# Performance work log

Hardware: AMD Instinct MI355X
Metric: run time of the kernel (lower is better)

The kernel has to match this reference:

```python
import math
import jax, jax.numpy as jnp
import numpy as np

B, NQ, NK, DIM, H, HD = 2, 1024, 2048, 1024, 16, 64


def setup_inputs() -> dict:
    key = jax.random.key(0)
    ks = jax.random.split(key, 12)
    s = 1.0 / math.sqrt(DIM)
    return {
        "q": jax.random.normal(ks[0], (B, NQ, DIM), jnp.float32),
        "k": jax.random.normal(ks[1], (B, NK, DIM), jnp.float32),
        "v": jax.random.normal(ks[2], (B, NK, DIM), jnp.float32),
        "distances": jax.random.uniform(ks[3], (B, NQ, NK), jnp.float32),
        "attn_mask": jax.random.bernoulli(ks[4], 0.5, (B, NQ, NK)),
        "key_padding_mask_q": jax.random.bernoulli(ks[5], 0.5, (B, NQ)),
        "key_padding_mask_k": jax.random.bernoulli(ks[6], 0.5, (B, NK)),
        "Wq": jax.random.normal(ks[7], (H * HD, DIM), jnp.float32) * s,
        "Wk": jax.random.normal(ks[8], (H * HD, DIM), jnp.float32) * s,
        "Wv": jax.random.normal(ks[9], (H * HD, DIM), jnp.float32) * s,
        "Wo": jax.random.normal(ks[10], (DIM, H * HD), jnp.float32) * s,
        "gate_alpha": jnp.float32(0.1),
    }


def reference(q, k, v, distances, attn_mask, key_padding_mask_q,
              key_padding_mask_k, Wq, Wk, Wv, Wo, gate_alpha):
    bsz, q_len, _ = q.shape
    k_len = k.shape[1]
    neg = jnp.finfo(q.dtype).min

    # projections -> (B, H, N, HD)
    qp = (q @ Wq.T).reshape(bsz, q_len, H, HD).transpose(0, 2, 1, 3)
    kp = (k @ Wk.T).reshape(bsz, k_len, H, HD).transpose(0, 2, 1, 3)
    vp = (v @ Wv.T).reshape(bsz, k_len, H, HD).transpose(0, 2, 1, 3)

    scores = jnp.einsum('bhqd,bhkd->bhqk', qp, kp) / math.sqrt(HD)
    scores = jnp.where(attn_mask[:, None, :, :], scores, neg)
    scores = jnp.where(key_padding_mask_k[:, None, None, :], scores, neg)

    attn = jax.nn.softmax(scores, axis=-1)  # (B,H,NQ,NK)

    # distance gating: mask, batch-mean normalize, exponential gate
    d = distances * attn_mask.astype(distances.dtype)
    d = d * key_padding_mask_k[:, None, :].astype(d.dtype)
    mean = d.sum(axis=(-1, -2)) / (q_len * k_len + 1e-6)
    mean = jnp.maximum(mean, 1e-6)[:, None, None]
    d = d / mean
    alpha = jax.nn.softplus(gate_alpha)
    gate = jnp.exp(-alpha * d)[:, None, :, :]  # (B,1,NQ,NK)

    w = attn * gate
    w = w / (w.sum(axis=-1, keepdims=True) + 1e-6)

    out = jnp.einsum('bhqk,bhkd->bhqd', w, vp)
    out = out.transpose(0, 2, 1, 3).reshape(bsz, q_len, H * HD)
    out = out * key_padding_mask_q[:, :, None].astype(out.dtype)
    return out @ Wo.T
```

## Files before the change

kernel.cpp:

```cpp
#include <hip/hip_runtime.h>
#include <hip/hip_bf16.h>
#include <cfloat>

#define B_   2
#define NQ_  1024
#define NK_  2048
#define H_   16
#define HD_  64
#define VPAD 2176
#define GPAD 2112

typedef float  floatx4 __attribute__((ext_vector_type(4)));
typedef __bf16 bf16x8  __attribute__((ext_vector_type(8)));
typedef __bf16 bf16x4  __attribute__((ext_vector_type(4)));

static __device__ __forceinline__ floatx4 mfma16(bf16x8 a, bf16x8 b, floatx4 c) {
    return __builtin_amdgcn_mfma_f32_16x16x32_bf16(a, b, c, 0, 0, 0);
}

static __device__ __forceinline__ void gl_lds(const __bf16* g, __bf16* lbase,
                                              int lane) {
#if __has_builtin(__builtin_amdgcn_global_load_lds)
    __builtin_amdgcn_global_load_lds(
        (const __attribute__((address_space(1))) void*)g,
        (__attribute__((address_space(3))) void*)lbase, 16, 0, 0);
#else
    *(bf16x8*)(lbase + lane * 8) = *(const bf16x8*)g;
#endif
}

struct CvtArgs {
    const float* src[7];
    __bf16*      dst[7];
};

__global__ __launch_bounds__(256) void cvt_mean_kernel(
    CvtArgs a, const float* __restrict__ dist, const int* __restrict__ amask,
    const int* __restrict__ kpmk, float* __restrict__ msum,
    __bf16* __restrict__ dmask)
{
    if (blockIdx.x >= 1792) {
        const int mb = blockIdx.x - 1792;
        const int b  = mb >> 9;
        const float* d  = dist  + (size_t)b * NQ_ * NK_;
        const int*   am = amask + (size_t)b * NQ_ * NK_;
        const int*   km = kpmk  + b * NK_;
        __bf16*      dm = dmask + (size_t)b * NQ_ * GPAD;
        const int base = (mb & 511) * 256 + threadIdx.x;
        float s = 0.f;
        #pragma unroll
        for (int j = 0; j < 4; j++) {
            const int i   = base + j * 131072;
            const int idx = i * 4;
            const int kk  = idx & (NK_ - 1);
            const int q   = i >> 9;
            float4 dv = *(const float4*)(d + idx);
            int4   mv = *(const int4*)(am + idx);
            int4   kv = *(const int4*)(km + kk);
            bf16x4 o;
            if (mv.x && kv.x) { s += dv.x; o[0] = (__bf16)dv.x; } else o[0] = (__bf16)3e38f;
            if (mv.y && kv.y) { s += dv.y; o[1] = (__bf16)dv.y; } else o[1] = (__bf16)3e38f;
            if (mv.z && kv.z) { s += dv.z; o[2] = (__bf16)dv.z; } else o[2] = (__bf16)3e38f;
            if (mv.w && kv.w) { s += dv.w; o[3] = (__bf16)dv.w; } else o[3] = (__bf16)3e38f;
            *(bf16x4*)&dm[(size_t)q * GPAD + kk] = o;
        }
        #pragma unroll
        for (int off = 32; off >= 1; off >>= 1) s += __shfl_down(s, off);
        __shared__ float wsum[4];
        if ((threadIdx.x & 63) == 0) wsum[threadIdx.x >> 6] = s;
        __syncthreads();
        if (threadIdx.x == 0)
            atomicAdd(&msum[b], wsum[0] + wsum[1] + wsum[2] + wsum[3]);
        return;
    }
    #pragma unroll
    for (int j = 0; j < 4; j++) {
        size_t r = (size_t)blockIdx.x * 1024 + j * 256 + threadIdx.x;
        int s;
        if (r < 262144)                  { s = 0; }
        else if ((r -= 262144) < 524288) { s = 1; }
        else if ((r -= 524288) < 524288) { s = 2; }
        else { r -= 524288; s = 3 + (int)(r >> 17); r &= 131071; }
        const float* sp = a.src[s] + r * 8;
        float4 f0 = *(const float4*)sp;
        float4 f1 = *(const float4*)(sp + 4);
        bf16x8 o;
        o[0] = (__bf16)f0.x; o[1] = (__bf16)f0.y; o[2] = (__bf16)f0.z; o[3] = (__bf16)f0.w;
        o[4] = (__bf16)f1.x; o[5] = (__bf16)f1.y; o[6] = (__bf16)f1.z; o[7] = (__bf16)f1.w;
        *(bf16x8*)(a.dst[s] + r * 8) = o;
    }
}

template <typename EPI>
static __device__ __forceinline__ void gemm128_core(
    const __bf16* __restrict__ A, const __bf16* __restrict__ Bw,
    int m0, int n0, __bf16* As, __bf16* Bs, EPI epi)
{
    const int t    = threadIdx.x;
    const int w    = t >> 6, lane = t & 63;
    const int lrow = lane & 15, quad = lane >> 4;
    const int lr   = lane >> 2, lc = lane & 3;

    floatx4 acc[4][4];
    #pragma unroll
    for (int mi = 0; mi < 4; mi++)
        #pragma unroll
        for (int ni = 0; ni < 4; ni++) acc[mi][ni] = floatx4{0.f, 0.f, 0.f, 0.f};

    const __bf16* ga = A  + (size_t)(m0 + w * 32 + lr) * 1024 + lc * 8;
    const __bf16* gb = Bw + (size_t)(n0 + w * 32 + lr) * 1024 + lc * 8;

    for (int k0 = 0; k0 < 1024; k0 += 64) {
        __syncthreads();
        #pragma unroll
        for (int h = 0; h < 2; h++) {
            gl_lds(ga + k0 + h * 32,             &As[h * 4096 + (w * 32) * 32],      lane);
            gl_lds(ga + k0 + h * 32 + 16 * 1024, &As[h * 4096 + (w * 32 + 16) * 32], lane);
            gl_lds(gb + k0 + h * 32,             &Bs[h * 4096 + (w * 32) * 32],      lane);
            gl_lds(gb + k0 + h * 32 + 16 * 1024, &Bs[h * 4096 + (w * 32 + 16) * 32], lane);
        }
        __syncthreads();

        #pragma unroll
        for (int h = 0; h < 2; h++) {
            bf16x8 af[4], bfr[4];
            #pragma unroll
            for (int mi = 0; mi < 4; mi++)
                af[mi] = *(const bf16x8*)
                    &As[h * 4096 + ((w & 1) * 64 + mi * 16 + lrow) * 32 + quad * 8];
            #pragma unroll
            for (int ni = 0; ni < 4; ni++)
                bfr[ni] = *(const bf16x8*)
                    &Bs[h * 4096 + ((w >> 1) * 64 + ni * 16 + lrow) * 32 + quad * 8];
            #pragma unroll
            for (int mi = 0; mi < 4; mi++)
                #pragma unroll
                for (int ni = 0; ni < 4; ni++)
                    acc[mi][ni] = mfma16(af[mi], bfr[ni], acc[mi][ni]);
        }
    }

    #pragma unroll
    for (int mi = 0; mi < 4; mi++)
        #pragma unroll
        for (int ni = 0; ni < 4; ni++)
            #pragma unroll
            for (int r = 0; r < 4; r++) {
                const int m = m0 + (w & 1) * 64 + mi * 16 + quad * 4 + r;
                const int n = n0 + (w >> 1) * 64 + ni * 16 + lrow;
                epi(m, n, acc[mi][ni][r]);
            }
}

template <typename EPI>
static __device__ __forceinline__ void gemm64_core(
    const __bf16* __restrict__ A, const __bf16* __restrict__ Bw,
    int m0, int n0, EPI epi)
{
    __shared__ alignas(16) __bf16 As[2][64 * 32];
    __shared__ alignas(16) __bf16 Bs[2][128 * 32];
    const int t    = threadIdx.x;
    const int w    = t >> 6, lane = t & 63;
    const int lrow = lane & 15, quad = lane >> 4;
    const int lr   = lane >> 2, lc = lane & 3;

    floatx4 acc[4][2];
    #pragma unroll
    for (int mi = 0; mi < 4; mi++)
        #pragma unroll
        for (int ni = 0; ni < 2; ni++) acc[mi][ni] = floatx4{0.f, 0.f, 0.f, 0.f};

    const __bf16* ga = A  + (size_t)(m0 + w * 16 + lr) * 1024 + lc * 8;
    const __bf16* gb = Bw + (size_t)(n0 + w * 32 + lr) * 1024 + lc * 8;

    for (int k0 = 0; k0 < 1024; k0 += 64) {
        __syncthreads();
        #pragma unroll
        for (int h = 0; h < 2; h++) {
            gl_lds(ga + k0 + h * 32,             &As[h][(w * 16) * 32],      lane);
            gl_lds(gb + k0 + h * 32,             &Bs[h][(w * 32) * 32],      lane);
            gl_lds(gb + k0 + h * 32 + 16 * 1024, &Bs[h][(w * 32 + 16) * 32], lane);
        }
        __syncthreads();

        #pragma unroll
        for (int h = 0; h < 2; h++) {
            bf16x8 af[4], bfr[2];
            #pragma unroll
            for (int mi = 0; mi < 4; mi++)
                af[mi] = *(const bf16x8*)
                    &As[h][(mi * 16 + lrow) * 32 + quad * 8];
            #pragma unroll
            for (int ni = 0; ni < 2; ni++)
                bfr[ni] = *(const bf16x8*)
                    &Bs[h][(w * 32 + ni * 16 + lrow) * 32 + quad * 8];
            #pragma unroll
            for (int mi = 0; mi < 4; mi++)
                #pragma unroll
                for (int ni = 0; ni < 2; ni++)
                    acc[mi][ni] = mfma16(af[mi], bfr[ni], acc[mi][ni]);
        }
    }

    #pragma unroll
    for (int mi = 0; mi < 4; mi++)
        #pragma unroll
        for (int ni = 0; ni < 2; ni++)
            #pragma unroll
            for (int r = 0; r < 4; r++) {
                const int m = m0 + mi * 16 + quad * 4 + r;
                const int n = n0 + w * 32 + ni * 16 + lrow;
                epi(m, n, acc[mi][ni][r]);
            }
}

__global__ __launch_bounds__(256) void proj_kernel(
    const __bf16* __restrict__ qb, const __bf16* __restrict__ kb,
    const __bf16* __restrict__ vb, const __bf16* __restrict__ wqb,
    const __bf16* __restrict__ wkb, const __bf16* __restrict__ wvb,
    __bf16* __restrict__ qp, __bf16* __restrict__ kp,
    __bf16* __restrict__ vpT)
{
    __shared__ alignas(16) __bf16 As[2 * 128 * 32];
    __shared__ alignas(16) __bf16 Bs[2 * 128 * 32];
    const int z = blockIdx.z;
    if (z == 0) {
        if ((int)blockIdx.x >= 16) return;
        gemm128_core(qb, wqb, blockIdx.x * 128, blockIdx.y * 128, As, Bs,
                     [&](int m, int n, float v) {
            const int b = m >> 10, q = m & 1023;
            const int h = n >> 6,  d = n & 63;
            qp[(((size_t)(b * 16 + h) * NQ_ + q) << 6) + d] = (__bf16)v;
        });
    } else if (z == 1) {
        gemm128_core(kb, wkb, blockIdx.x * 128, blockIdx.y * 128, As, Bs,
                     [&](int m, int n, float v) {
            const int b = m >> 11, key = m & 2047;
            const int h = n >> 6,  d = n & 63;
            kp[(((size_t)(b * 16 + h) * NK_ + key) << 6) + d] = (__bf16)v;
        });
    } else {
        gemm128_core(wvb, vb, blockIdx.y * 128, blockIdx.x * 128, As, Bs,
                     [&](int m, int n, float v) {
            const int h = m >> 6,  d = m & 63;
            const int b = n >> 11, key = n & 2047;
            vpT[((size_t)(b * 16 + h) * HD_ + d) * VPAD + key] = (__bf16)v;
        });
    }
}

__global__ __launch_bounds__(256) void oproj_kernel(
    const __bf16* __restrict__ A, const __bf16* __restrict__ W,
    float* __restrict__ Cout)
{
    const int m0 = blockIdx.x * 64, n0 = blockIdx.y * 128;
    gemm64_core(A, W, m0, n0, [&](int m, int n, float v) {
        Cout[(size_t)m * 1024 + n] = v;
    });
}

__global__ __launch_bounds__(512, 4) void attn_kernel(
    const __bf16* __restrict__ qp, const __bf16* __restrict__ kp,
    const __bf16* __restrict__ vpT, const __bf16* __restrict__ dmask,
    const float* __restrict__ msum, const float* __restrict__ galpha,
    const int* __restrict__ kpmq, __bf16* __restrict__ attnout)
{
    __shared__ __bf16 Ks[2][64 * 72];
    __shared__ __bf16 Vt[2][64 * 72];
    __shared__ __bf16 Ps[8][16 * 72];
    __shared__ float  Ox[4][16][68];
    __shared__ float  Gx[4][16];
    const int t    = threadIdx.x;
    const int w    = t >> 6, lane = t & 63;
    const int g    = w >> 2;
    const int wg   = w & 3;
    const int lrow = lane & 15, quad = lane >> 4;
    const int qt   = blockIdx.x;
    const int bh   = blockIdx.y;
    const int b    = bh >> 4, h = bh & 15;
    const int q0   = qt * 64 + wg * 16;
    const int k0   = g * (NK_ / 2);
    const int NT   = (NK_ / 2) / 64;

    const float mean  = fmaxf(msum[b] / ((float)(NQ_ * NK_) + 1e-6f), 1e-6f);
    const float alpha = log1pf(__expf(galpha[0]));
    const float cg    = -alpha / mean;

    const __bf16* qb = qp + ((size_t)bh * NQ_ + q0 + lrow) * HD_ + quad * 8;
    const bf16x8 qf0 = *(const bf16x8*)qb;
    const bf16x8 qf1 = *(const bf16x8*)(qb + 32);

    const int tg    = t & 255;
    const int srow0 = tg >> 3,        sc0 = tg & 7;
    const int srow1 = 32 + (tg >> 3), sc1 = tg & 7;
    const int so0 = srow0 * 72 + sc0 * 8;
    const int so1 = srow1 * 72 + sc1 * 8;
    const __bf16* Kg = kp  + (size_t)bh * NK_ * HD_;
    const __bf16* Vg = vpT + (size_t)bh * HD_ * VPAD;
    const __bf16* grow = dmask + ((size_t)b * NQ_ + q0 + lrow) * GPAD;

    float G = 0.f;
    floatx4 O[4];
    #pragma unroll
    for (int nb = 0; nb < 4; nb++) O[nb] = floatx4{0.f, 0.f, 0.f, 0.f};

    bf16x8 kr0, kr1, vr0, vr1;
    bf16x4 gr[4];
    auto loadt = [&](int kb) {
        kr0 = *(const bf16x8*)(Kg + (size_t)(kb + srow0) * HD_ + sc0 * 8);
        kr1 = *(const bf16x8*)(Kg + (size_t)(kb + srow1) * HD_ + sc1 * 8);
        vr0 = *(const bf16x8*)(Vg + (size_t)srow0 * VPAD + kb + sc0 * 8);
        vr1 = *(const bf16x8*)(Vg + (size_t)srow1 * VPAD + kb + sc1 * 8);
        #pragma unroll
        for (int c = 0; c < 4; c++)
            gr[c] = *(const bf16x4*)(grow + kb + c * 16 + quad * 4);
    };
    loadt(k0);

    for (int ib = 0; ib < NT; ib++) {
        const int kb = k0 + ib * 64;

        __syncthreads();
        *(bf16x8*)&Ks[g][so0] = kr0;
        *(bf16x8*)&Ks[g][so1] = kr1;
        *(bf16x8*)&Vt[g][so0] = vr0;
        *(bf16x8*)&Vt[g][so1] = vr1;
        __syncthreads();

        bf16x4 gcur[4];
        #pragma unroll
        for (int c = 0; c < 4; c++) gcur[c] = gr[c];
        if (ib + 1 < NT) loadt(kb + 64);

        floatx4 s4[4];
        #pragma unroll
        for (int c = 0; c < 4; c++) {
            bf16x8 kf0 = *(const bf16x8*)&Ks[g][(c * 16 + lrow) * 72 + quad * 8];
            bf16x8 kf1 = *(const bf16x8*)&Ks[g][(c * 16 + lrow) * 72 + 32 + quad * 8];
            floatx4 a = floatx4{0.f, 0.f, 0.f, 0.f};
            a = mfma16(kf0, qf0, a);
            a = mfma16(kf1, qf1, a);
            s4[c] = a;
        }

        #pragma unroll
        for (int c = 0; c < 4; c++) {
            const float e0 = __expf(fmaf(s4[c][0], 0.125f, cg * (float)gcur[c][0]));
            const float e1 = __expf(fmaf(s4[c][1], 0.125f, cg * (float)gcur[c][1]));
            const float e2 = __expf(fmaf(s4[c][2], 0.125f, cg * (float)gcur[c][2]));
            const float e3 = __expf(fmaf(s4[c][3], 0.125f, cg * (float)gcur[c][3]));
            G += (e0 + e1) + (e2 + e3);
            bf16x4 pk;
            pk[0] = (__bf16)e0; pk[1] = (__bf16)e1;
            pk[2] = (__bf16)e2; pk[3] = (__bf16)e3;
            *(bf16x4*)&Ps[w][lrow * 72 + c * 16 + quad * 4] = pk;
        }

        {
            bf16x8 pf0 = *(const bf16x8*)&Ps[w][lrow * 72 + quad * 8];
            bf16x8 pf1 = *(const bf16x8*)&Ps[w][lrow * 72 + 32 + quad * 8];
            #pragma unroll
            for (int nb = 0; nb < 4; nb++) {
                bf16x8 vf0 = *(const bf16x8*)
                    &Vt[g][(nb * 16 + lrow) * 72 + quad * 8];
                bf16x8 vf1 = *(const bf16x8*)
                    &Vt[g][(nb * 16 + lrow) * 72 + 32 + quad * 8];
                O[nb] = mfma16(pf0, vf0, O[nb]);
                O[nb] = mfma16(pf1, vf1, O[nb]);
            }
        }
    }

    G += __shfl_xor(G, 16);
    G += __shfl_xor(G, 32);

    __syncthreads();
    if (g == 1) {
        #pragma unroll
        for (int nb = 0; nb < 4; nb++)
            #pragma unroll
            for (int r = 0; r < 4; r++)
                Ox[wg][quad * 4 + r][nb * 16 + lrow] = O[nb][r];
        if (quad == 0) Gx[wg][lrow] = G;
    }
    __syncthreads();
    if (g == 0) {
        #pragma unroll
        for (int r = 0; r < 4; r++) {
            const int j  = quad * 4 + r;
            const int q  = q0 + j;
            const float gq = __shfl(G, j) + Gx[wg][j];
            const float f  = kpmq[b * NQ_ + q] ? 1.f / (gq + 1e-30f) : 0.f;
            #pragma unroll
            for (int nb = 0; nb < 4; nb++) {
                const float ov = O[nb][r] + Ox[wg][j][nb * 16 + lrow];
                attnout[((size_t)b * NQ_ + q) * 1024 + h * HD_ + nb * 16 + lrow] =
                    (__bf16)(ov * f);
            }
        }
    }
}

extern "C" void kernel_launch(void* const* d_in, const int* in_sizes, int n_in,
                              void* d_out, int out_size, void* d_ws,
                              size_t ws_size, hipStream_t stream)
{
    const float* q      = (const float*)d_in[0];
    const float* k      = (const float*)d_in[1];
    const float* v      = (const float*)d_in[2];
    const float* dist   = (const float*)d_in[3];
    const int*   amask  = (const int*)d_in[4];
    const int*   kpmq   = (const int*)d_in[5];
    const int*   kpmk   = (const int*)d_in[6];
    const float* Wq     = (const float*)d_in[7];
    const float* Wk     = (const float*)d_in[8];
    const float* Wv     = (const float*)d_in[9];
    const float* Wo     = (const float*)d_in[10];
    const float* galpha = (const float*)d_in[11];

    char* p = (char*)d_ws;
    float*  msum = (float*)p;                 p += 256;
    __bf16* qb   = (__bf16*)p;                p += (size_t)2097152 * 2;
    __bf16* kb   = (__bf16*)p;                p += (size_t)4194304 * 2;
    __bf16* vb   = (__bf16*)p;                p += (size_t)4194304 * 2;
    __bf16* wqb  = (__bf16*)p;                p += (size_t)1048576 * 2;
    __bf16* wkb  = (__bf16*)p;                p += (size_t)1048576 * 2;
    __bf16* wvb  = (__bf16*)p;                p += (size_t)1048576 * 2;
    __bf16* wob  = (__bf16*)p;                p += (size_t)1048576 * 2;
    __bf16* qp   = (__bf16*)p;                p += (size_t)2097152 * 2;
    __bf16* kpb  = (__bf16*)p;                p += (size_t)4194304 * 2;
    __bf16* vpT  = (__bf16*)p;                p += (size_t)32 * 64 * VPAD * 2;
    __bf16* dmask = (__bf16*)p;               p += (size_t)2048 * GPAD * 2;
    __bf16* attnout = (__bf16*)p;             p += (size_t)2097152 * 2;

    CvtArgs ca;
    ca.src[0] = q;  ca.src[1] = k;  ca.src[2] = v;
    ca.src[3] = Wq; ca.src[4] = Wk; ca.src[5] = Wv; ca.src[6] = Wo;
    ca.dst[0] = qb;  ca.dst[1] = kb;  ca.dst[2] = vb;
    ca.dst[3] = wqb; ca.dst[4] = wkb; ca.dst[5] = wvb; ca.dst[6] = wob;

    hipMemsetAsync(msum, 0, 256, stream);
    cvt_mean_kernel<<<2816, 256, 0, stream>>>(ca, dist, amask, kpmk, msum,
                                              dmask);
    proj_kernel<<<dim3(32, 8, 3), 256, 0, stream>>>(qb, kb, vb, wqb, wkb, wvb,
                                                    qp, kpb, vpT);
    attn_kernel<<<dim3(16, 32), 512, 0, stream>>>(qp, kpb, vpT, dmask,
                                                  msum, galpha, kpmq, attnout);
    oproj_kernel<<<dim3(32, 8), 256, 0, stream>>>(attnout, wob, (float*)d_out);
}
```

Measured before the change: 248.2 us.

## Process two 16-row query groups per wave in attention to reuse K/V tiles

Each wave now handles 32 query rows instead of 16, so every K and V fragment loaded from LDS feeds two MFMAs, and each block covers 128 queries. The grid is halved to 8x32 blocks. The P staging buffer and the cross-group output reduction buffer now share one LDS region, and launch bounds drop to 2 blocks per CU to make room for the extra registers. The aim is to cut LDS traffic and global K/V reloads per unit of work. The cost is higher register pressure and only 256 blocks, which may underfill the CUs.

```diff
diff --git a/kernel.cpp b/kernel.cpp
--- a/kernel.cpp
+++ b/kernel.cpp
@@ -259,7 +259,7 @@
     });
 }
 
-__global__ __launch_bounds__(512, 4) void attn_kernel(
+__global__ __launch_bounds__(512, 2) void attn_kernel(
     const __bf16* __restrict__ qp, const __bf16* __restrict__ kp,
     const __bf16* __restrict__ vpT, const __bf16* __restrict__ dmask,
     const float* __restrict__ msum, const float* __restrict__ galpha,
@@ -267,9 +267,8 @@
 {
     __shared__ __bf16 Ks[2][64 * 72];
     __shared__ __bf16 Vt[2][64 * 72];
-    __shared__ __bf16 Ps[8][16 * 72];
-    __shared__ float  Ox[4][16][68];
-    __shared__ float  Gx[4][16];
+    __shared__ alignas(16) char PsOx[8 * 32 * 72 * 2];
+    __shared__ float  Gx[4][32];
     const int t    = threadIdx.x;
     const int w    = t >> 6, lane = t & 63;
     const int g    = w >> 2;
@@ -278,17 +277,25 @@
     const int qt   = blockIdx.x;
     const int bh   = blockIdx.y;
     const int b    = bh >> 4, h = bh & 15;
-    const int q0   = qt * 64 + wg * 16;
+    const int q0   = qt * 128 + wg * 32;
     const int k0   = g * (NK_ / 2);
     const int NT   = (NK_ / 2) / 64;
+
+    __bf16* Ps = (__bf16*)PsOx + w * 32 * 72;
+    float (*Ox)[32][68] = (float (*)[32][68])PsOx;
 
     const float mean  = fmaxf(msum[b] / ((float)(NQ_ * NK_) + 1e-6f), 1e-6f);
     const float alpha = log1pf(__expf(galpha[0]));
     const float cg    = -alpha / mean;
 
-    const __bf16* qb = qp + ((size_t)bh * NQ_ + q0 + lrow) * HD_ + quad * 8;
-    const bf16x8 qf0 = *(const bf16x8*)qb;
-    const bf16x8 qf1 = *(const bf16x8*)(qb + 32);
+    bf16x8 qf[2][2];
+    #pragma unroll
+    for (int qg = 0; qg < 2; qg++) {
+        const __bf16* qb = qp + ((size_t)bh * NQ_ + q0 + qg * 16 + lrow) * HD_ +
+                           quad * 8;
+        qf[qg][0] = *(const bf16x8*)qb;
+        qf[qg][1] = *(const bf16x8*)(qb + 32);
+    }
 
     const int tg    = t & 255;
     const int srow0 = tg >> 3,        sc0 = tg & 7;
@@ -297,23 +304,31 @@
     const int so1 = srow1 * 72 + sc1 * 8;
     const __bf16* Kg = kp  + (size_t)bh * NK_ * HD_;
     const __bf16* Vg = vpT + (size_t)bh * HD_ * VPAD;
-    const __bf16* grow = dmask + ((size_t)b * NQ_ + q0 + lrow) * GPAD;
-
-    float G = 0.f;
-    floatx4 O[4];
-    #pragma unroll
-    for (int nb = 0; nb < 4; nb++) O[nb] = floatx4{0.f, 0.f, 0.f, 0.f};
+
+    const __bf16* grow[2];
+    #pragma unroll
+    for (int qg = 0; qg < 2; qg++)
+        grow[qg] = dmask + ((size_t)b * NQ_ + q0 + qg * 16 + lrow) * GPAD;
+
+    float G[2] = {0.f, 0.f};
+    floatx4 O[2][4];
+    #pragma unroll
+    for (int qg = 0; qg < 2; qg++)
+        #pragma unroll
+        for (int nb = 0; nb < 4; nb++) O[qg][nb] = floatx4{0.f, 0.f, 0.f, 0.f};
 
     bf16x8 kr0, kr1, vr0, vr1;
-    bf16x4 gr[4];
+    bf16x4 gr[2][4];
     auto loadt = [&](int kb) {
         kr0 = *(const bf16x8*)(Kg + (size_t)(kb + srow0) * HD_ + sc0 * 8);
         kr1 = *(const bf16x8*)(Kg + (size_t)(kb + srow1) * HD_ + sc1 * 8);
         vr0 = *(const bf16x8*)(Vg + (size_t)srow0 * VPAD + kb + sc0 * 8);
         vr1 = *(const bf16x8*)(Vg + (size_t)srow1 * VPAD + kb + sc1 * 8);
         #pragma unroll
-        for (int c = 0; c < 4; c++)
-            gr[c] = *(const bf16x4*)(grow + kb + c * 16 + quad * 4);
+        for (int qg = 0; qg < 2; qg++)
+            #pragma unroll
+            for (int c = 0; c < 4; c++)
+                gr[qg][c] = *(const bf16x4*)(grow[qg] + kb + c * 16 + quad * 4);
     };
     loadt(k0);
 
@@ -327,75 +342,98 @@
         *(bf16x8*)&Vt[g][so1] = vr1;
         __syncthreads();
 
-        bf16x4 gcur[4];
-        #pragma unroll
-        for (int c = 0; c < 4; c++) gcur[c] = gr[c];
+        bf16x4 gcur[2][4];
+        #pragma unroll
+        for (int qg = 0; qg < 2; qg++)
+            #pragma unroll
+            for (int c = 0; c < 4; c++) gcur[qg][c] = gr[qg][c];
         if (ib + 1 < NT) loadt(kb + 64);
 
-        floatx4 s4[4];
+        floatx4 s4[2][4];
         #pragma unroll
         for (int c = 0; c < 4; c++) {
             bf16x8 kf0 = *(const bf16x8*)&Ks[g][(c * 16 + lrow) * 72 + quad * 8];
             bf16x8 kf1 = *(const bf16x8*)&Ks[g][(c * 16 + lrow) * 72 + 32 + quad * 8];
-            floatx4 a = floatx4{0.f, 0.f, 0.f, 0.f};
-            a = mfma16(kf0, qf0, a);
-            a = mfma16(kf1, qf1, a);
-            s4[c] = a;
-        }
-
-        #pragma unroll
-        for (int c = 0; c < 4; c++) {
-            const float e0 = __expf(fmaf(s4[c][0], 0.125f, cg * (float)gcur[c][0]));
-            const float e1 = __expf(fmaf(s4[c][1], 0.125f, cg * (float)gcur[c][1]));
-            const float e2 = __expf(fmaf(s4[c][2], 0.125f, cg * (float)gcur[c][2]));
-            const float e3 = __expf(fmaf(s4[c][3], 0.125f, cg * (float)gcur[c][3]));
-            G += (e0 + e1) + (e2 + e3);
-            bf16x4 pk;
-            pk[0] = (__bf16)e0; pk[1] = (__bf16)e1;
-            pk[2] = (__bf16)e2; pk[3] = (__bf16)e3;
-            *(bf16x4*)&Ps[w][lrow * 72 + c * 16 + quad * 4] = pk;
-        }
-
-        {
-            bf16x8 pf0 = *(const bf16x8*)&Ps[w][lrow * 72 + quad * 8];
-            bf16x8 pf1 = *(const bf16x8*)&Ps[w][lrow * 72 + 32 + quad * 8];
+            #pragma unroll
+            for (int qg = 0; qg < 2; qg++) {
+                floatx4 a = floatx4{0.f, 0.f, 0.f, 0.f};
+                a = mfma16(kf0, qf[qg][0], a);
+                a = mfma16(kf1, qf[qg][1], a);
+                s4[qg][c] = a;
+            }
+        }
+
+        #pragma unroll
+        for (int qg = 0; qg < 2; qg++) {
+            #pragma unroll
+            for (int c = 0; c < 4; c++) {
+                const float e0 = __expf(fmaf(s4[qg][c][0], 0.125f, cg * (float)gcur[qg][c][0]));
+                const float e1 = __expf(fmaf(s4[qg][c][1], 0.125f, cg * (float)gcur[qg][c][1]));
+                const float e2 = __expf(fmaf(s4[qg][c][2], 0.125f, cg * (float)gcur[qg][c][2]));
+                const float e3 = __expf(fmaf(s4[qg][c][3], 0.125f, cg * (float)gcur[qg][c][3]));
+                G[qg] += (e0 + e1) + (e2 + e3);
+                bf16x4 pk;
+                pk[0] = (__bf16)e0; pk[1] = (__bf16)e1;
+                pk[2] = (__bf16)e2; pk[3] = (__bf16)e3;
+                *(bf16x4*)&Ps[(qg * 16 + lrow) * 72 + c * 16 + quad * 4] = pk;
+            }
+        }
+
+        bf16x8 pf[2][2];
+        #pragma unroll
+        for (int qg = 0; qg < 2; qg++) {
+            pf[qg][0] = *(const bf16x8*)&Ps[(qg * 16 + lrow) * 72 + quad * 8];
+            pf[qg][1] = *(const bf16x8*)&Ps[(qg * 16 + lrow) * 72 + 32 + quad * 8];
+        }
+        #pragma unroll
+        for (int tt = 0; tt < 2; tt++)
             #pragma unroll
             for (int nb = 0; nb < 4; nb++) {
-                bf16x8 vf0 = *(const bf16x8*)
-                    &Vt[g][(nb * 16 + lrow) * 72 + quad * 8];
-                bf16x8 vf1 = *(const bf16x8*)
-                    &Vt[g][(nb * 16 + lrow) * 72 + 32 + quad * 8];
-                O[nb] = mfma16(pf0, vf0, O[nb]);
-                O[nb] = mfma16(pf1, vf1, O[nb]);
-            }
-        }
-    }
-
-    G += __shfl_xor(G, 16);
-    G += __shfl_xor(G, 32);
+                bf16x8 vf = *(const bf16x8*)
+                    &Vt[g][(nb * 16 + lrow) * 72 + tt * 32 + quad * 8];
+                #pragma unroll
+                for (int qg = 0; qg < 2; qg++)
+                    O[qg][nb] = mfma16(pf[qg][tt], vf, O[qg][nb]);
+            }
+    }
+
+    #pragma unroll
+    for (int qg = 0; qg < 2; qg++) {
+        G[qg] += __shfl_xor(G[qg], 16);
+        G[qg] += __shfl_xor(G[qg], 32);
+    }
 
     __syncthreads();
     if (g == 1) {
         #pragma unroll
-        for (int nb = 0; nb < 4; nb++)
-            #pragma unroll
-            for (int r = 0; r < 4; r++)
-                Ox[wg][quad * 4 + r][nb * 16 + lrow] = O[nb][r];
-        if (quad == 0) Gx[wg][lrow] = G;
+        for (int qg = 0; qg < 2; qg++)
+            #pragma unroll
+            for (int nb = 0; nb < 4; nb++)
+                #pragma unroll
+                for (int r = 0; r < 4; r++)
+                    Ox[wg][qg * 16 + quad * 4 + r][nb * 16 + lrow] = O[qg][nb][r];
+        if (quad == 0) {
+            #pragma unroll
+            for (int qg = 0; qg < 2; qg++)
+                Gx[wg][qg * 16 + lrow] = G[qg];
+        }
     }
     __syncthreads();
     if (g == 0) {
         #pragma unroll
-        for (int r = 0; r < 4; r++) {
-            const int j  = quad * 4 + r;
-            const int q  = q0 + j;
-            const float gq = __shfl(G, j) + Gx[wg][j];
-            const float f  = kpmq[b * NQ_ + q] ? 1.f / (gq + 1e-30f) : 0.f;
-            #pragma unroll
-            for (int nb = 0; nb < 4; nb++) {
-                const float ov = O[nb][r] + Ox[wg][j][nb * 16 + lrow];
-                attnout[((size_t)b * NQ_ + q) * 1024 + h * HD_ + nb * 16 + lrow] =
-                    (__bf16)(ov * f);
+        for (int qg = 0; qg < 2; qg++) {
+            #pragma unroll
+            for (int r = 0; r < 4; r++) {
+                const int j  = qg * 16 + quad * 4 + r;
+                const int q  = q0 + j;
+                const float gq = __shfl(G[qg], quad * 4 + r) + Gx[wg][j];
+                const float f  = kpmq[b * NQ_ + q] ? 1.f / (gq + 1e-30f) : 0.f;
+                #pragma unroll
+                for (int nb = 0; nb < 4; nb++) {
+                    const float ov = O[qg][nb][r] + Ox[wg][j][nb * 16 + lrow];
+                    attnout[((size_t)b * NQ_ + q) * 1024 + h * HD_ + nb * 16 + lrow] =
+                        (__bf16)(ov * f);
+                }
             }
         }
     }
@@ -444,7 +482,7 @@
                                               dmask);
     proj_kernel<<<dim3(32, 8, 3), 256, 0, stream>>>(qb, kb, vb, wqb, wkb, wvb,
                                                     qp, kpb, vpT);
-    attn_kernel<<<dim3(16, 32), 512, 0, stream>>>(qp, kpb, vpT, dmask,
-                                                  msum, galpha, kpmq, attnout);
+    attn_kernel<<<dim3(8, 32), 512, 0, stream>>>(qp, kpb, vpT, dmask,
+                                                 msum, galpha, kpmq, attnout);
     oproj_kernel<<<dim3(32, 8), 256, 0, stream>>>(attnout, wob, (float*)d_out);
 }
```

After: 261.2 us. +5.2%, slower.
